# Performance work log

Measured on AMD Instinct MI355X. Metric: run time of the kernel, lower is better.

The kernel has to match this reference:

```python
import jax, jax.numpy as jnp
import numpy as np

B, S, D, H = 2, 2048, 1024, 16
DK = D // H


def setup_inputs() -> dict:
    key = jax.random.key(0)
    ks = jax.random.split(key, 12)
    scale = 1.0 / np.sqrt(D)
    inp = {
        "q": jax.random.normal(ks[0], (B, S, D), jnp.float32),
        "k": jax.random.normal(ks[1], (B, S, D), jnp.float32),
        "v": jax.random.normal(ks[2], (B, S, D), jnp.float32),
        "mask": jax.random.randint(ks[3], (B, 1, S, S), 0, 2, jnp.int32),
        "w_q": jax.random.normal(ks[4], (D, D), jnp.float32) * scale,
        "b_q": jnp.zeros((D,), jnp.float32),
        "w_k": jax.random.normal(ks[5], (D, D), jnp.float32) * scale,
        "b_k": jnp.zeros((D,), jnp.float32),
        "w_v": jax.random.normal(ks[6], (D, D), jnp.float32) * scale,
        "b_v": jnp.zeros((D,), jnp.float32),
        "w_o": jax.random.normal(ks[7], (D, D), jnp.float32) * scale,
        "b_o": jnp.zeros((D,), jnp.float32),
    }
    return inp


def reference(q, k, v, mask, w_q, b_q, w_k, b_k, w_v, b_v, w_o, b_o):
    # linear projections (torch Linear: x @ W.T + b)
    qp = q @ w_q.T + b_q  # [B,S,D]
    kp = k @ w_k.T + b_k
    vp = v @ w_v.T + b_v
    # split heads -> [B,H,S,DK]
    qh = qp.reshape(B, S, H, DK).transpose(0, 2, 1, 3)
    kh = kp.reshape(B, S, H, DK).transpose(0, 2, 1, 3)
    vh = vp.reshape(B, S, H, DK).transpose(0, 2, 1, 3)
    # scaled dot-product attention
    scores = jnp.einsum("bhqd,bhkd->bhqk", qh, kh) / jnp.sqrt(jnp.float32(DK))
    scores = jnp.where(mask == 0, jnp.float32(-1e9), scores)
    attn = jax.nn.softmax(scores, axis=-1)
    ctx = jnp.einsum("bhqk,bhkd->bhqd", attn, vh)  # [B,H,S,DK]
    ctx = ctx.transpose(0, 2, 1, 3).reshape(B, S, D)
    return ctx @ w_o.T + b_o
```

## Files before the change

kernel.cpp:

```cpp
#include <hip/hip_runtime.h>
#include <hip/hip_bf16.h>
#include <cstdint>

#define DEVINL __device__ __forceinline__

using bfrag = __attribute__((ext_vector_type(8))) __bf16;
using f32x4 = __attribute__((ext_vector_type(4))) float;
using f32x16 = __attribute__((ext_vector_type(16))) float;
using u16x4 = __attribute__((ext_vector_type(4))) unsigned short;
using u16x8 = __attribute__((ext_vector_type(8))) unsigned short;
using u32x4 = __attribute__((ext_vector_type(4))) unsigned int;

static constexpr int S_ = 2048;
static constexpr int D_ = 1024;
static constexpr int MROWS = 4096;

DEVINL unsigned short f2bf(float f) {
  __hip_bfloat16 h = __float2bfloat16(f);
  union { __hip_bfloat16 h; unsigned short u; } cv; cv.h = h; return cv.u;
}

DEVINL float fexp2(float x) {
#if __has_builtin(__builtin_amdgcn_exp2f)
  return __builtin_amdgcn_exp2f(x);
#else
  return exp2f(x);
#endif
}

DEVINL unsigned cvtpk(float lo, float hi) {
  unsigned r;
  asm("v_cvt_pk_bf16_f32 %0, %1, %2" : "=v"(r) : "v"(lo), "v"(hi));
  return r;
}

DEVINL void plswap(unsigned& x, unsigned& y) {
#if __has_builtin(__builtin_amdgcn_permlane32_swap)
  auto r = __builtin_amdgcn_permlane32_swap(x, y, false, false);
  x = r[0]; y = r[1];
#else
  unsigned px = __shfl_xor(x, 32), py = __shfl_xor(y, 32);
  bool h = (threadIdx.x & 32) != 0;
  unsigned nx = h ? py : x;
  unsigned ny = h ? y : px;
  x = nx; y = ny;
#endif
}

DEVINL void async_copy16(void* lds, const void* g) {
  __builtin_amdgcn_global_load_lds(
      (const __attribute__((address_space(1))) unsigned int*)g,
      (__attribute__((address_space(3))) unsigned int*)lds, 16, 0, 0);
}

struct CvtW {
  const float* src[4];
  unsigned short* dst[4];
  const int* mask;
  unsigned long long* bits;
  int nmask;
};

__global__ __launch_bounds__(256) void cvt_w(CvtW a) {
  if (blockIdx.y == 4) {
    const int n = a.nmask;
    for (int i = blockIdx.x * 256 + threadIdx.x; i < n; i += gridDim.x * 256) {
      unsigned long long b = __ballot(a.mask[i] != 0);
      if ((threadIdx.x & 63) == 0) a.bits[i >> 6] = b;
    }
    return;
  }
  const float* __restrict__ in = a.src[blockIdx.y];
  unsigned short* __restrict__ out = a.dst[blockIdx.y];
  const int n4 = D_ * D_ / 4;
  for (int i = blockIdx.x * 256 + threadIdx.x; i < n4; i += gridDim.x * 256) {
    f32x4 v = ((const f32x4*)in)[i];
    u16x4 o;
    o[0] = f2bf(v[0]); o[1] = f2bf(v[1]); o[2] = f2bf(v[2]); o[3] = f2bf(v[3]);
    ((u16x4*)out)[i] = o;
  }
}

template <int OMODE>
DEVINL void gemm_body_f32A(const float* __restrict__ Af, const unsigned short* __restrict__ W,
                           const float* __restrict__ bias, void* __restrict__ Cout,
                           float oscale, char* AsB, char* BsB, int m0, int n0) {
  constexpr int K = D_, N = D_;
  const int t = threadIdx.x;
  const int lane = t & 63, wave = t >> 6;
  const int wr = wave >> 1, wc = wave & 1;
  const int g = lane >> 4, q = lane & 15;

  f32x4 acc[4][4] = {};

  const int srow = t >> 3;
  const int sgz = (t & 7) ^ (srow & 7);
  const int arow = ((t >> 6) & 3) * 4 + ((t >> 4) & 3);
  const int agz = ((t & 15) ^ ((((t >> 6) & 1) << 2) | ((t >> 4) & 3))) * 4;

  for (int k0 = 0; k0 < K; k0 += 64) {
    __syncthreads();
#pragma unroll
    for (int c = 0; c < 4; ++c)
      async_copy16(BsB + c * 4096 + wave * 1024,
                   W + (size_t)(n0 + c * 32 + srow) * K + k0 + sgz * 8);
#pragma unroll
    for (int c = 0; c < 8; ++c)
      async_copy16(AsB + c * 4096 + wave * 1024,
                   Af + (size_t)(m0 + c * 16 + arow) * K + k0 + agz);
    __syncthreads();
#pragma unroll
    for (int kk = 0; kk < 64; kk += 32) {
      bfrag af[4], bf[4];
#pragma unroll
      for (int i = 0; i < 4; ++i) {
        const int ar = wr * 64 + i * 16 + q;
        const char* Ar = AsB + ar * 256;
        const int gi = (kk >> 2) + 2 * g;
        f32x4 v0 = *reinterpret_cast<const f32x4*>(Ar + ((gi ^ (q & 7)) << 4));
        f32x4 v1 = *reinterpret_cast<const f32x4*>(Ar + (((gi + 1) ^ (q & 7)) << 4));
        u32x4 wv;
        wv[0] = cvtpk(v0[0], v0[1]); wv[1] = cvtpk(v0[2], v0[3]);
        wv[2] = cvtpk(v1[0], v1[1]); wv[3] = cvtpk(v1[2], v1[3]);
        af[i] = __builtin_bit_cast(bfrag, wv);
      }
#pragma unroll
      for (int j = 0; j < 4; ++j) {
        const int br = wc * 64 + j * 16 + q;
        bf[j] = *reinterpret_cast<const bfrag*>(
            BsB + br * 128 + ((((kk >> 3) + g) ^ (q & 7)) << 4));
      }
#pragma unroll
      for (int i = 0; i < 4; ++i)
#pragma unroll
        for (int j = 0; j < 4; ++j)
          acc[i][j] = __builtin_amdgcn_mfma_f32_16x16x32_bf16(af[i], bf[j], acc[i][j], 0, 0, 0);
    }
  }

  float bv[4];
#pragma unroll
  for (int j = 0; j < 4; ++j) bv[j] = bias[n0 + wc * 64 + j * 16 + q];
#pragma unroll
  for (int i = 0; i < 4; ++i)
#pragma unroll
    for (int j = 0; j < 4; ++j) {
      int rowb = m0 + wr * 64 + i * 16 + g * 4;
      int col = n0 + wc * 64 + j * 16 + q;
      if (OMODE == 2) {
        u16x4 o;
#pragma unroll
        for (int r = 0; r < 4; ++r) o[r] = f2bf(acc[i][j][r] + bv[j]);
        *reinterpret_cast<u16x4*>(&((unsigned short*)Cout)[(size_t)col * MROWS + rowb]) = o;
      } else {
#pragma unroll
        for (int r = 0; r < 4; ++r) {
          float val = (acc[i][j][r] + bv[j]) * oscale;
          ((unsigned short*)Cout)[(size_t)(rowb + r) * N + col] = f2bf(val);
        }
      }
    }
}

__global__ __launch_bounds__(256, 2) void qkv_gemm(const float* __restrict__ Aq,
                                                   const float* __restrict__ Ak,
                                                   const float* __restrict__ Av,
                                                   const unsigned short* __restrict__ Wbase,
                                                   const float* __restrict__ b_q,
                                                   const float* __restrict__ b_k,
                                                   const float* __restrict__ b_v,
                                                   unsigned short* __restrict__ Qp,
                                                   unsigned short* __restrict__ Kp,
                                                   unsigned short* __restrict__ VpT) {
  __shared__ char As[128 * 64 * 4];
  __shared__ char Bs[128 * 64 * 2];
  const int lin = blockIdx.x + 8 * (blockIdx.y + 32 * blockIdx.z);
  const int tile = (lin & 7) * 96 + (lin >> 3);
  const int bx = tile & 7, by = (tile >> 3) & 31, z = tile >> 8;
  const unsigned short* W = Wbase + (size_t)z * D_ * D_;
  const int m0 = by * 128, n0 = bx * 128;
  if (z == 2) {
    gemm_body_f32A<2>(Av, W, b_v, VpT, 1.0f, As, Bs, m0, n0);
  } else if (z == 1) {
    gemm_body_f32A<0>(Ak, W, b_k, Kp, 1.0f, As, Bs, m0, n0);
  } else {
    gemm_body_f32A<0>(Aq, W, b_q, Qp, 0.125f * 1.44269504088896340736f, As, Bs, m0, n0);
  }
}

__global__ __launch_bounds__(256, 2) void out_gemm(const unsigned short* __restrict__ A,
                                                   const unsigned short* __restrict__ W,
                                                   const float* __restrict__ bias,
                                                   float* __restrict__ out) {
  __shared__ char As[2 * 128 * 64 * 2];
  __shared__ char Bs[2 * 128 * 64 * 2];
  constexpr int K = D_, N = D_, NK = K / 64;
  const int lin = blockIdx.x + 8 * blockIdx.y;
  const int tile = (lin & 7) * 32 + (lin >> 3);
  const int bx = tile & 7, by = tile >> 3;
  const int m0 = by * 128, n0 = bx * 128;

  const int t = threadIdx.x;
  const int lane = t & 63, wave = t >> 6;
  const int wr = wave >> 1, wc = wave & 1;
  const int g = lane >> 4, q = lane & 15;
  const int srow = t >> 3;
  const int sgz = (t & 7) ^ (srow & 7);

  f32x4 acc[4][4] = {};

  auto stage = [&](int buf, int k0) {
#pragma unroll
    for (int c = 0; c < 4; ++c) {
      async_copy16(As + buf * 16384 + c * 4096 + wave * 1024,
                   A + (size_t)(m0 + c * 32 + srow) * K + k0 + sgz * 8);
      async_copy16(Bs + buf * 16384 + c * 4096 + wave * 1024,
                   W + (size_t)(n0 + c * 32 + srow) * K + k0 + sgz * 8);
    }
  };

  stage(0, 0);
  __syncthreads();

#pragma unroll 1
  for (int ki = 0; ki < NK; ++ki) {
    const int cur = ki & 1;
    if (ki + 1 < NK) stage(cur ^ 1, (ki + 1) * 64);
#pragma unroll
    for (int kk = 0; kk < 64; kk += 32) {
      bfrag af[4], bf[4];
#pragma unroll
      for (int i = 0; i < 4; ++i)
        af[i] = *reinterpret_cast<const bfrag*>(
            As + cur * 16384 + (wr * 64 + i * 16 + q) * 128 + ((((kk >> 3) + g) ^ (q & 7)) << 4));
#pragma unroll
      for (int j = 0; j < 4; ++j)
        bf[j] = *reinterpret_cast<const bfrag*>(
            Bs + cur * 16384 + (wc * 64 + j * 16 + q) * 128 + ((((kk >> 3) + g) ^ (q & 7)) << 4));
#pragma unroll
      for (int i = 0; i < 4; ++i)
#pragma unroll
        for (int j = 0; j < 4; ++j)
          acc[i][j] = __builtin_amdgcn_mfma_f32_16x16x32_bf16(af[i], bf[j], acc[i][j], 0, 0, 0);
    }
    __syncthreads();
  }

  float bv[4];
#pragma unroll
  for (int j = 0; j < 4; ++j) bv[j] = bias[n0 + wc * 64 + j * 16 + q];
#pragma unroll
  for (int i = 0; i < 4; ++i)
#pragma unroll
    for (int j = 0; j < 4; ++j)
#pragma unroll
      for (int r = 0; r < 4; ++r) {
        int row = m0 + wr * 64 + i * 16 + g * 4 + r;
        int col = n0 + wc * 64 + j * 16 + q;
        out[(size_t)row * N + col] = acc[i][j][r] + bv[j];
      }
}

__global__ __launch_bounds__(256, 2) void attn_kernel(const unsigned short* __restrict__ Qp,
                                                      const unsigned short* __restrict__ Kp,
                                                      const unsigned short* __restrict__ VpT,
                                                      const unsigned int* __restrict__ mbits32,
                                                      unsigned short* __restrict__ ctx) {
  __shared__ unsigned short Ks[2][128 * 64];
  __shared__ unsigned short Vt[2][64 * 128];

  const int t = threadIdx.x, lane = t & 63, wave = t >> 6;
  const int hi = lane >> 5, qh = lane & 31;
  const int id = blockIdx.x + 16 * (blockIdx.y + 16 * blockIdx.z);
  const int tile = (id & 7) * 64 + (id >> 3);
  const int qt = tile & 15, bh = tile >> 4;
  const int h = bh & 15, b = bh >> 4;
  const int q0 = qt * 128;
  const int qrow = q0 + wave * 32 + qh;

  const size_t qoff = ((size_t)b * S_ + qrow) * D_ + h * 64;
  bfrag qf[4];
#pragma unroll
  for (int ks = 0; ks < 4; ++ks)
    qf[ks] = *reinterpret_cast<const bfrag*>(&Qp[qoff + ks * 16 + hi * 8]);

  f32x16 acc_o[2] = {};
  f32x16 acc_l = {};

  u16x8 onesv;
#pragma unroll
  for (int j = 0; j < 8; ++j) onesv[j] = 0x3F80;
  const bfrag ones = __builtin_bit_cast(bfrag, onesv);

  const int krow = wave * 8 + (lane >> 3);
  const int ksc = ((lane & 7) ^ (lane >> 3)) * 8;
  const size_t kbase = (size_t)b * S_ * D_ + (size_t)h * 64;
  const int vrow = wave * 4 + (lane >> 4);
  const int vsc = ((lane & 15) ^ (vrow & 7)) * 8;
  const size_t vtrow0 = (size_t)h * 64;
  const size_t vtcol0 = (size_t)b * S_;

  char* KsB = (char*)&Ks[0][0];
  char* VtB = (char*)&Vt[0][0];
  const unsigned int* mrow = mbits32 + ((size_t)b * S_ + qrow) * (S_ / 32);
  const int swz = qh & 7;

  constexpr int NT = S_ / 128;

  auto stage = [&](int buf, int ti) {
#pragma unroll
    for (int c = 0; c < 4; ++c)
      async_copy16(KsB + buf * 16384 + c * 4096 + wave * 1024,
                   &Kp[kbase + (size_t)(ti * 128 + c * 32 + krow) * D_ + ksc]);
#pragma unroll
    for (int c = 0; c < 4; ++c)
      async_copy16(VtB + buf * 16384 + c * 4096 + wave * 1024,
                   &VpT[(vtrow0 + c * 16 + vrow) * MROWS + vtcol0 + ti * 128 + vsc]);
  };

  stage(0, 0);
  __syncthreads();

  auto tile_body = [&](int ti, int cur) {
    const int nxt = cur ^ 1;
    if (ti + 1 < NT) stage(nxt, ti + 1);
    u32x4 m4 = *reinterpret_cast<const u32x4*>(mrow + ti * 4);

    f32x16 sc[4];
    const f32x16 fz = {};
    __builtin_amdgcn_s_setprio(1);
#pragma unroll
    for (int kb = 0; kb < 4; ++kb) {
#pragma unroll
      for (int ks = 0; ks < 4; ++ks) {
        bfrag kf = *reinterpret_cast<const bfrag*>(
            KsB + cur * 16384 + (kb * 32 + qh) * 128 + ((((2 * ks + hi) ^ swz) & 7) << 4));
        sc[kb] = __builtin_amdgcn_mfma_f32_32x32x16_bf16(kf, qf[ks], ks == 0 ? fz : sc[kb], 0, 0, 0);
      }
    }
    __builtin_amdgcn_s_setprio(0);

    const int sh4 = 4 * hi;
#pragma unroll
    for (int kb = 0; kb < 4; ++kb) {
      unsigned w = m4[kb] >> sh4;
#pragma unroll
      for (int g2 = 0; g2 < 4; ++g2) {
        unsigned nib = (w >> (8 * g2)) & 0xFu;
#pragma unroll
        for (int r3 = 0; r3 < 4; ++r3) {
          float p = fexp2(sc[kb][g2 * 4 + r3]);
          sc[kb][g2 * 4 + r3] = (nib & (1u << r3)) ? p : 0.f;
        }
      }
    }

    bfrag pa[8];
#pragma unroll
    for (int ks = 0; ks < 8; ++ks) {
      const int o = ks * 8;
      unsigned a1 = cvtpk(sc[(o + 0) >> 4][(o + 0) & 15], sc[(o + 1) >> 4][(o + 1) & 15]);
      unsigned a2 = cvtpk(sc[(o + 2) >> 4][(o + 2) & 15], sc[(o + 3) >> 4][(o + 3) & 15]);
      unsigned b1 = cvtpk(sc[(o + 4) >> 4][(o + 4) & 15], sc[(o + 5) >> 4][(o + 5) & 15]);
      unsigned b2 = cvtpk(sc[(o + 6) >> 4][(o + 6) & 15], sc[(o + 7) >> 4][(o + 7) & 15]);
      plswap(a1, b1);
      plswap(a2, b2);
      u32x4 wv; wv[0] = a1; wv[1] = a2; wv[2] = b1; wv[3] = b2;
      pa[ks] = __builtin_bit_cast(bfrag, wv);
    }

    __builtin_amdgcn_s_setprio(1);
#pragma unroll
    for (int ks = 0; ks < 8; ++ks) {
      acc_l = __builtin_amdgcn_mfma_f32_32x32x16_bf16(ones, pa[ks], acc_l, 0, 0, 0);
#pragma unroll
      for (int dblk = 0; dblk < 2; ++dblk) {
        bfrag va = *reinterpret_cast<const bfrag*>(
            VtB + cur * 16384 + (dblk * 32 + qh) * 256 + ((((2 * ks + hi) ^ swz) & 15) << 4));
        acc_o[dblk] = __builtin_amdgcn_mfma_f32_32x32x16_bf16(va, pa[ks], acc_o[dblk], 0, 0, 0);
      }
    }
    __builtin_amdgcn_s_setprio(0);
    __syncthreads();
  };

#pragma unroll 1
  for (int ti = 0; ti < NT; ti += 2) {
    tile_body(ti, 0);
    tile_body(ti + 1, 1);
  }

  float inv = 1.f / acc_l[0];
#pragma unroll
  for (int dblk = 0; dblk < 2; ++dblk)
#pragma unroll
    for (int g2 = 0; g2 < 4; ++g2) {
      u16x4 o;
#pragma unroll
      for (int r3 = 0; r3 < 4; ++r3) o[r3] = f2bf(acc_o[dblk][g2 * 4 + r3] * inv);
      int d0 = dblk * 32 + 8 * g2 + 4 * hi;
      *reinterpret_cast<u16x4*>(&ctx[((size_t)b * S_ + qrow) * D_ + h * 64 + d0]) = o;
    }
}

extern "C" void kernel_launch(void* const* d_in, const int* in_sizes, int n_in,
                              void* d_out, int out_size, void* d_ws, size_t ws_size,
                              hipStream_t stream) {
  const float* q = (const float*)d_in[0];
  const float* k = (const float*)d_in[1];
  const float* v = (const float*)d_in[2];
  const int* mask = (const int*)d_in[3];
  const float* w_q = (const float*)d_in[4];
  const float* b_q = (const float*)d_in[5];
  const float* w_k = (const float*)d_in[6];
  const float* b_k = (const float*)d_in[7];
  const float* w_v = (const float*)d_in[8];
  const float* b_v = (const float*)d_in[9];
  const float* w_o = (const float*)d_in[10];
  const float* b_o = (const float*)d_in[11];
  float* out = (float*)d_out;

  char* ws = (char*)d_ws;
  const size_t SZ_IN = (size_t)MROWS * D_ * 2;
  const size_t SZ_W = (size_t)D_ * D_ * 2;
  unsigned short* wqb = (unsigned short*)(ws + 3 * SZ_IN);
  unsigned short* wob = (unsigned short*)(ws + 3 * SZ_IN + 3 * SZ_W);
  unsigned short* Qp = (unsigned short*)(ws + 3 * SZ_IN + 4 * SZ_W);
  unsigned short* ctx = (unsigned short*)(ws + 6 * SZ_IN + 4 * SZ_W);
  unsigned long long* mbits = (unsigned long long*)(ws + 7 * SZ_IN + 4 * SZ_W);
  unsigned short* wkb = wqb + D_ * D_;
  unsigned short* wvb = wkb + D_ * D_;
  unsigned short* Kp = Qp + MROWS * D_;
  unsigned short* VpT = Kp + MROWS * D_;

  CvtW cw;
  cw.src[0] = w_q; cw.dst[0] = wqb;
  cw.src[1] = w_k; cw.dst[1] = wkb;
  cw.src[2] = w_v; cw.dst[2] = wvb;
  cw.src[3] = w_o; cw.dst[3] = wob;
  cw.mask = mask; cw.bits = mbits; cw.nmask = 2 * S_ * S_;
  cvt_w<<<dim3(1024, 5), 256, 0, stream>>>(cw);

  qkv_gemm<<<dim3(D_ / 128, MROWS / 128, 3), 256, 0, stream>>>(q, k, v, wqb, b_q, b_k, b_v,
                                                               Qp, Kp, VpT);

  attn_kernel<<<dim3(S_ / 128, 16, 2), 256, 0, stream>>>(Qp, Kp, VpT,
                                                         (const unsigned int*)mbits, ctx);

  out_gemm<<<dim3(D_ / 128, MROWS / 128), 256, 0, stream>>>(ctx, wob, b_o, out);
}
```

Baseline: 127.5 us.

## Triple-buffer QKV projection GEMM with async prefetch two stages ahead

Rewrites the QKV GEMM main loop to use a K-step of 32 with three LDS buffers, issuing async global-to-LDS copies two iterations ahead and waiting with explicit vmcnt counters and a single barrier per step. This replaces the previous load-then-compute pattern with two barriers per 64-wide K step, so global load latency can overlap MFMA work. LDS use grows from 48KB to 72KB per block, which may reduce occupancy below the declared two blocks per CU, and it relies on hand-written waitcnt values matching the copy count.

```diff
diff --git a/kernel.cpp b/kernel.cpp
--- a/kernel.cpp
+++ b/kernel.cpp
@@ -82,10 +82,10 @@
 }
 
 template <int OMODE>
-DEVINL void gemm_body_f32A(const float* __restrict__ Af, const unsigned short* __restrict__ W,
-                           const float* __restrict__ bias, void* __restrict__ Cout,
-                           float oscale, char* AsB, char* BsB, int m0, int n0) {
-  constexpr int K = D_, N = D_;
+DEVINL void gemm_cnt(const float* __restrict__ Af, const unsigned short* __restrict__ W,
+                     const float* __restrict__ bias, void* __restrict__ Cout,
+                     float oscale, char* AsB, char* BsB, int m0, int n0) {
+  constexpr int K = D_, N = D_, NK = K / 32;
   const int t = threadIdx.x;
   const int lane = t & 63, wave = t >> 6;
   const int wr = wave >> 1, wc = wave & 1;
@@ -93,49 +93,65 @@
 
   f32x4 acc[4][4] = {};
 
-  const int srow = t >> 3;
-  const int sgz = (t & 7) ^ (srow & 7);
-  const int arow = ((t >> 6) & 3) * 4 + ((t >> 4) & 3);
-  const int agz = ((t & 15) ^ ((((t >> 6) & 1) << 2) | ((t >> 4) & 3))) * 4;
-
-  for (int k0 = 0; k0 < K; k0 += 64) {
-    __syncthreads();
-#pragma unroll
-    for (int c = 0; c < 4; ++c)
-      async_copy16(BsB + c * 4096 + wave * 1024,
-                   W + (size_t)(n0 + c * 32 + srow) * K + k0 + sgz * 8);
-#pragma unroll
-    for (int c = 0; c < 8; ++c)
-      async_copy16(AsB + c * 4096 + wave * 1024,
-                   Af + (size_t)(m0 + c * 16 + arow) * K + k0 + agz);
-    __syncthreads();
-#pragma unroll
-    for (int kk = 0; kk < 64; kk += 32) {
-      bfrag af[4], bf[4];
-#pragma unroll
-      for (int i = 0; i < 4; ++i) {
-        const int ar = wr * 64 + i * 16 + q;
-        const char* Ar = AsB + ar * 256;
-        const int gi = (kk >> 2) + 2 * g;
-        f32x4 v0 = *reinterpret_cast<const f32x4*>(Ar + ((gi ^ (q & 7)) << 4));
-        f32x4 v1 = *reinterpret_cast<const f32x4*>(Ar + (((gi + 1) ^ (q & 7)) << 4));
-        u32x4 wv;
-        wv[0] = cvtpk(v0[0], v0[1]); wv[1] = cvtpk(v0[2], v0[3]);
-        wv[2] = cvtpk(v1[0], v1[1]); wv[3] = cvtpk(v1[2], v1[3]);
-        af[i] = __builtin_bit_cast(bfrag, wv);
-      }
-#pragma unroll
-      for (int j = 0; j < 4; ++j) {
-        const int br = wc * 64 + j * 16 + q;
-        bf[j] = *reinterpret_cast<const bfrag*>(
-            BsB + br * 128 + ((((kk >> 3) + g) ^ (q & 7)) << 4));
-      }
-#pragma unroll
-      for (int i = 0; i < 4; ++i)
-#pragma unroll
-        for (int j = 0; j < 4; ++j)
-          acc[i][j] = __builtin_amdgcn_mfma_f32_16x16x32_bf16(af[i], bf[j], acc[i][j], 0, 0, 0);
-    }
+  const int asrow = t >> 3;
+  const int agz = (t & 7) ^ (asrow & 7);
+  const int bsrow = t >> 2;
+  const int bgz = (t & 3) ^ (bsrow & 3);
+
+  auto stage = [&](int buf, int ki) {
+    const int k0 = ki * 32;
+#pragma unroll
+    for (int l = 0; l < 4; ++l)
+      async_copy16(AsB + buf * 16384 + l * 4096 + wave * 1024,
+                   Af + (size_t)(m0 + l * 32 + asrow) * K + k0 + agz * 4);
+#pragma unroll
+    for (int l = 0; l < 2; ++l)
+      async_copy16(BsB + buf * 8192 + l * 4096 + wave * 1024,
+                   W + (size_t)(n0 + l * 64 + bsrow) * K + k0 + bgz * 8);
+  };
+
+  auto compute = [&](int buf) {
+    bfrag af[4], bf[4];
+#pragma unroll
+    for (int i = 0; i < 4; ++i) {
+      const int ar = wr * 64 + i * 16 + q;
+      const char* Ar = AsB + buf * 16384 + ar * 128;
+      f32x4 v0 = *reinterpret_cast<const f32x4*>(Ar + (((2 * g + 0) ^ (q & 7)) << 4));
+      f32x4 v1 = *reinterpret_cast<const f32x4*>(Ar + (((2 * g + 1) ^ (q & 7)) << 4));
+      u32x4 wv;
+      wv[0] = cvtpk(v0[0], v0[1]); wv[1] = cvtpk(v0[2], v0[3]);
+      wv[2] = cvtpk(v1[0], v1[1]); wv[3] = cvtpk(v1[2], v1[3]);
+      af[i] = __builtin_bit_cast(bfrag, wv);
+    }
+#pragma unroll
+    for (int j = 0; j < 4; ++j) {
+      const int br = wc * 64 + j * 16 + q;
+      bf[j] = *reinterpret_cast<const bfrag*>(
+          BsB + buf * 8192 + br * 64 + ((g ^ (br & 3)) << 4));
+    }
+#pragma unroll
+    for (int i = 0; i < 4; ++i)
+#pragma unroll
+      for (int j = 0; j < 4; ++j)
+        acc[i][j] = __builtin_amdgcn_mfma_f32_16x16x32_bf16(af[i], bf[j], acc[i][j], 0, 0, 0);
+  };
+
+  stage(0, 0);
+  stage(1, 1);
+  asm volatile("s_waitcnt vmcnt(6)" ::: "memory");
+  __builtin_amdgcn_s_barrier();
+  __builtin_amdgcn_sched_barrier(0);
+
+#pragma unroll 1
+  for (int ki = 0; ki < NK; ++ki) {
+    if (ki + 2 < NK) stage((ki + 2) % 3, ki + 2);
+    compute(ki % 3);
+    if (ki + 2 < NK)
+      asm volatile("s_waitcnt vmcnt(6)" ::: "memory");
+    else
+      asm volatile("s_waitcnt vmcnt(0)" ::: "memory");
+    __builtin_amdgcn_s_barrier();
+    __builtin_amdgcn_sched_barrier(0);
   }
 
   float bv[4];
@@ -172,19 +188,19 @@
                                                    unsigned short* __restrict__ Qp,
                                                    unsigned short* __restrict__ Kp,
                                                    unsigned short* __restrict__ VpT) {
-  __shared__ char As[128 * 64 * 4];
-  __shared__ char Bs[128 * 64 * 2];
+  __shared__ char As[3 * 16384];
+  __shared__ char Bs[3 * 8192];
   const int lin = blockIdx.x + 8 * (blockIdx.y + 32 * blockIdx.z);
   const int tile = (lin & 7) * 96 + (lin >> 3);
   const int bx = tile & 7, by = (tile >> 3) & 31, z = tile >> 8;
   const unsigned short* W = Wbase + (size_t)z * D_ * D_;
   const int m0 = by * 128, n0 = bx * 128;
   if (z == 2) {
-    gemm_body_f32A<2>(Av, W, b_v, VpT, 1.0f, As, Bs, m0, n0);
+    gemm_cnt<2>(Av, W, b_v, VpT, 1.0f, As, Bs, m0, n0);
   } else if (z == 1) {
-    gemm_body_f32A<0>(Ak, W, b_k, Kp, 1.0f, As, Bs, m0, n0);
+    gemm_cnt<0>(Ak, W, b_k, Kp, 1.0f, As, Bs, m0, n0);
   } else {
-    gemm_body_f32A<0>(Aq, W, b_q, Qp, 0.125f * 1.44269504088896340736f, As, Bs, m0, n0);
+    gemm_cnt<0>(Aq, W, b_q, Qp, 0.125f * 1.44269504088896340736f, As, Bs, m0, n0);
   }
 }
 
```

Result: slower. 150.7 us (+18.2%).
